# Kernel optimization log

Hardware: AMD Instinct MI355X
Metric: run time of the kernel (lower is better)

## Reference

```python
import jax, jax.numpy as jnp
import numpy as np

NUM_TYPES = 4
EPS = 1e-5
NEG_SLOPE = 0.01  # nn.LeakyReLU default


def hetero_linear(x, node_type, W, b):
    # x: [N, Cin], W: [T, Cin, Cout], b: [T, Cout]
    # Grouped GEMM via type-masked batched matmul (T is small and fixed).
    onehot = jax.nn.one_hot(node_type, NUM_TYPES, dtype=x.dtype)  # [N, T]
    xt = onehot.T[:, :, None] * x[None, :, :]                      # [T, N, Cin]
    y = jnp.einsum('tni,tio->no', xt, W)                           # [N, Cout]
    return y + b[node_type]


def hetero_batchnorm(x, node_type, gamma, beta):
    # Per-type batch statistics over the nodes of each type (training-mode BN).
    ones = jnp.ones((x.shape[0],), dtype=x.dtype)
    cnt = jax.ops.segment_sum(ones, node_type, num_segments=NUM_TYPES)      # [T]
    cnt = jnp.maximum(cnt, 1.0)
    s = jax.ops.segment_sum(x, node_type, num_segments=NUM_TYPES)           # [T, C]
    ss = jax.ops.segment_sum(x * x, node_type, num_segments=NUM_TYPES)      # [T, C]
    mean = s / cnt[:, None]
    var = ss / cnt[:, None] - mean * mean  # biased variance, as BN uses
    xn = (x - mean[node_type]) * jax.lax.rsqrt(var[node_type] + EPS)
    return xn * gamma[node_type] + beta[node_type]


def setup_inputs() -> dict:
    key = jax.random.key(0)
    ks = jax.random.split(key, 12)
    N, CIN, H, COUT, T = 32768, 256, 512, 256, NUM_TYPES
    x = jax.random.normal(ks[0], (N, CIN), dtype=jnp.float32)
    node_type = jax.random.randint(ks[1], (N,), 0, T, dtype=jnp.int32)
    def lin(k, ci, co):
        k1, k2 = jax.random.split(k)
        scale = 1.0 / np.sqrt(ci)
        W = jax.random.uniform(k1, (T, ci, co), jnp.float32, -scale, scale)
        b = jax.random.uniform(k2, (T, co), jnp.float32, -scale, scale)
        return W, b
    W1, b1 = lin(ks[2], CIN, H)
    W2, b2 = lin(ks[3], H, H)
    W3, b3 = lin(ks[4], H, COUT)
    gamma1 = jnp.ones((T, H), jnp.float32)
    beta1 = jnp.zeros((T, H), jnp.float32)
    gamma2 = jnp.ones((T, H), jnp.float32)
    beta2 = jnp.zeros((T, H), jnp.float32)
    return {"x": x, "node_type": node_type,
            "W1": W1, "b1": b1, "W2": W2, "b2": b2, "W3": W3, "b3": b3,
            "gamma1": gamma1, "beta1": beta1, "gamma2": gamma2, "beta2": beta2}


def reference(x, node_type, W1, b1, W2, b2, W3, b3, gamma1, beta1, gamma2, beta2):
    # Layer 1: HeteroLinear -> HeteroBatchNorm -> LeakyReLU (dropout p=0 -> identity)
    h = hetero_linear(x, node_type, W1, b1)
    h = hetero_batchnorm(h, node_type, gamma1, beta1)
    h = jax.nn.leaky_relu(h, NEG_SLOPE)
    # Layer 2
    h = hetero_linear(h, node_type, W2, b2)
    h = hetero_batchnorm(h, node_type, gamma2, beta2)
    h = jax.nn.leaky_relu(h, NEG_SLOPE)
    # Layer 3: plain_last -> no norm/act
    out = hetero_linear(h, node_type, W3, b3)
    return out
```

## Files before the change

### kernel.cpp

```cpp
#include <hip/hip_runtime.h>
#include <cstdint>
#include <cstddef>

#define N_NODES 32768
#define CIN 256
#define HDIM 512
#define COUT_F 256
#define NTYPE 4
#define ALIGN_SEG 128
#define NPAD (N_NODES + NTYPE * ALIGN_SEG)
#define BN_EPS 1e-5f
#define SLOPE 0.01f
#define NCHUNK 64

typedef unsigned short u16;
typedef __attribute__((ext_vector_type(8))) short bf16x8;
typedef __attribute__((ext_vector_type(4))) float f32x4;
typedef __attribute__((ext_vector_type(4))) u16 u16x4;

#define GLOBAL_AS __attribute__((address_space(1)))
#define LDS_AS __attribute__((address_space(3)))

__device__ __forceinline__ u16 f2bf(float f) {
  union { float f; unsigned u; } v{f};
  unsigned r = (v.u + 0x7FFF + ((v.u >> 16) & 1)) >> 16;
  return (u16)r;
}


__global__ void hist_kernel(const int* __restrict__ nt, int* __restrict__ blockHist) {
  __shared__ int h[NTYPE];
  int tid = threadIdx.x;
  if (tid < NTYPE) h[tid] = 0;
  __syncthreads();
  int i = blockIdx.x * 256 + tid;
  atomicAdd(&h[nt[i]], 1);
  __syncthreads();
  if (tid < NTYPE) blockHist[blockIdx.x * NTYPE + tid] = h[tid];
}

__global__ void scan_kernel(const int* __restrict__ blockHist, int* __restrict__ blockBase,
                            int* __restrict__ meta) {
  int tid = threadIdx.x;
  if (tid < NTYPE) {
    int run = 0;
    for (int b = 0; b < 128; ++b) {
      blockBase[b * NTYPE + tid] = run;
      run += blockHist[b * NTYPE + tid];
    }
    meta[tid] = run;
  }
  __syncthreads();
  if (tid == 0) {
    int s = 0;
    for (int t = 0; t < NTYPE; ++t) {
      meta[4 + t] = s;
      s += (meta[t] + ALIGN_SEG - 1) & ~(ALIGN_SEG - 1);
    }
    meta[8] = s;
  }
}

__global__ void rank_scatter_kernel(const int* __restrict__ nt, const int* __restrict__ blockBase,
                                    const int* __restrict__ meta, int* __restrict__ perm) {
  __shared__ int st[256];
  int tid = threadIdx.x;
  int i = blockIdx.x * 256 + tid;
  int t = nt[i];
  st[tid] = t;
  __syncthreads();
  int rank = 0;
  for (int j = 0; j < tid; ++j) rank += (st[j] == t) ? 1 : 0;
  perm[meta[4 + t] + blockBase[blockIdx.x * NTYPE + t] + rank] = i;
}

__global__ void gather_kernel(const float* __restrict__ x, const int* __restrict__ perm,
                              u16* __restrict__ xs) {
  int p = blockIdx.x;
  int src = perm[p];
  u16x4* dst = (u16x4*)(xs + (size_t)p * CIN);
  if (src < 0) {
    dst[threadIdx.x] = (u16x4)0;
  } else {
    float4 v = ((const float4*)(x + (size_t)src * CIN))[threadIdx.x];
    u16x4 o;
    o.x = f2bf(v.x); o.y = f2bf(v.y); o.z = f2bf(v.z); o.w = f2bf(v.w);
    dst[threadIdx.x] = o;
  }
}

template <int K, int COUT>
__global__ __launch_bounds__(256) void wtrans_kernel(const float* __restrict__ W,
                                                     u16* __restrict__ Wt) {
  const int t = blockIdx.z;
  const int k0 = blockIdx.x * 32, c0 = blockIdx.y * 32;
  const float* __restrict__ Ws = W + (size_t)t * K * COUT;
  u16* __restrict__ Wd = Wt + (size_t)t * COUT * K;
  __shared__ float tile[32][33];
  int tid = threadIdx.x;
#pragma unroll
  for (int p = 0; p < 4; ++p) {
    int idx = p * 256 + tid;
    int r = idx >> 5, c = idx & 31;
    tile[r][c] = Ws[(size_t)(k0 + r) * COUT + c0 + c];
  }
  __syncthreads();
#pragma unroll
  for (int p = 0; p < 4; ++p) {
    int idx = p * 256 + tid;
    int r = idx >> 5, c = idx & 31;
    Wd[(size_t)(c0 + r) * K + k0 + c] = f2bf(tile[c][r]);
  }
}


template <int K, int COUT, bool SCATTER>
__global__ __launch_bounds__(256) void mfma_gemm_kernel(
    const u16* __restrict__ A, const u16* __restrict__ Wt, const float* __restrict__ bias,
    float* __restrict__ Y, const int* __restrict__ meta, const int* __restrict__ perm) {
  const int col0 = blockIdx.x * 128, row0 = blockIdx.y * 128;
  const int s1 = meta[5], s2 = meta[6], s3 = meta[7];
  const int t = row0 >= s3 ? 3 : (row0 >= s2 ? 2 : (row0 >= s1 ? 1 : 0));
  const u16* __restrict__ Bt = Wt + (size_t)t * COUT * K;

  __shared__ __align__(16) u16 As[128 * 32];
  __shared__ __align__(16) u16 Bs[128 * 32];

  const int tid = threadIdx.x;
  const int wid = tid >> 6, lane = tid & 63;
  const int lr = lane & 15, ls = lane >> 4;
  const int wm = wid >> 1, wn = wid & 1;

  int a_off[4], b_off[4];
#pragma unroll
  for (int i = 0; i < 4; ++i) {
    int r = wm * 64 + i * 16 + lr;
    a_off[i] = r * 32 + (ls ^ ((r >> 1) & 3)) * 8;
  }
#pragma unroll
  for (int j = 0; j < 4; ++j) {
    int r = wn * 64 + j * 16 + lr;
    b_off[j] = r * 32 + (ls ^ ((r >> 1) & 3)) * 8;
  }

  int st_row[2], st_k[2];
#pragma unroll
  for (int p = 0; p < 2; ++p) {
    int c = p * 256 + tid;
    int r = c >> 2;
    int s = (c & 3) ^ ((r >> 1) & 3);
    st_row[p] = r;
    st_k[p] = s * 8;
  }
  const int lds_base0 = (tid & 192) * 8;

  f32x4 acc[4][4] = {};

  for (int k0 = 0; k0 < K; k0 += 32) {
#pragma unroll
    for (int p = 0; p < 2; ++p) {
      const u16* ga = A + (size_t)(row0 + st_row[p]) * K + k0 + st_k[p];
      const u16* gb = Bt + (size_t)(col0 + st_row[p]) * K + k0 + st_k[p];
      u16* la = As + p * 2048 + lds_base0;
      u16* lb = Bs + p * 2048 + lds_base0;
      __builtin_amdgcn_global_load_lds((const GLOBAL_AS void*)ga, (LDS_AS void*)la, 16, 0, 0);
      __builtin_amdgcn_global_load_lds((const GLOBAL_AS void*)gb, (LDS_AS void*)lb, 16, 0, 0);
    }
    __syncthreads();
    bf16x8 af[4], bfr[4];
#pragma unroll
    for (int i = 0; i < 4; ++i) af[i] = *(const bf16x8*)(As + a_off[i]);
#pragma unroll
    for (int j = 0; j < 4; ++j) bfr[j] = *(const bf16x8*)(Bs + b_off[j]);
#pragma unroll
    for (int i = 0; i < 4; ++i)
#pragma unroll
      for (int j = 0; j < 4; ++j)
        acc[i][j] = __builtin_amdgcn_mfma_f32_16x16x32_bf16(af[i], bfr[j], acc[i][j], 0, 0, 0);
    __syncthreads();
  }

  float bj[4];
#pragma unroll
  for (int j = 0; j < 4; ++j) bj[j] = bias[(size_t)t * COUT + col0 + wn * 64 + j * 16 + lr];

#pragma unroll
  for (int i = 0; i < 4; ++i) {
    int rbase = row0 + wm * 64 + i * 16 + ls * 4;
    if (SCATTER) {
      int dsts[4];
#pragma unroll
      for (int r = 0; r < 4; ++r) dsts[r] = perm[rbase + r];
#pragma unroll
      for (int j = 0; j < 4; ++j) {
        int gcol = col0 + wn * 64 + j * 16 + lr;
#pragma unroll
        for (int r = 0; r < 4; ++r) {
          if (dsts[r] >= 0) Y[(size_t)dsts[r] * COUT + gcol] = acc[i][j][r] + bj[j];
        }
      }
    } else {
#pragma unroll
      for (int j = 0; j < 4; ++j) {
        int gcol = col0 + wn * 64 + j * 16 + lr;
#pragma unroll
        for (int r = 0; r < 4; ++r) {
          Y[(size_t)(rbase + r) * COUT + gcol] = acc[i][j][r] + bj[j];
        }
      }
    }
  }
}


__global__ __launch_bounds__(256) void bn_partial_kernel(const float* __restrict__ h,
                                                         const int* __restrict__ meta,
                                                         float* __restrict__ partS,
                                                         float* __restrict__ partQ) {
  const int t = blockIdx.y;
  const int chunk = blockIdx.z;
  const int lane = threadIdx.x & 63;
  const int rl = threadIdx.x >> 6;
  const int c = blockIdx.x * 64 + lane;
  const int start = meta[4 + t];
  const int cnt = meta[t];
  float s = 0.f, q = 0.f;
  for (int r = chunk * 4 + rl; r < cnt; r += NCHUNK * 4) {
    float v = h[(size_t)(start + r) * HDIM + c];
    s += v;
    q += v * v;
  }
  __shared__ float redS[4][64], redQ[4][64];
  redS[rl][lane] = s;
  redQ[rl][lane] = q;
  __syncthreads();
  if (rl == 0) {
    float S = redS[0][lane] + redS[1][lane] + redS[2][lane] + redS[3][lane];
    float Q = redQ[0][lane] + redQ[1][lane] + redQ[2][lane] + redQ[3][lane];
    size_t o = ((size_t)t * NCHUNK + chunk) * HDIM + c;
    partS[o] = S;
    partQ[o] = Q;
  }
}

__global__ __launch_bounds__(256) void bn_finalize_kernel(const float* __restrict__ partS,
                                                          const float* __restrict__ partQ,
                                                          const int* __restrict__ meta,
                                                          float* __restrict__ mean,
                                                          float* __restrict__ rstd) {
  int idx = blockIdx.x * 256 + threadIdx.x;
  int t = idx >> 9;
  int c = idx & (HDIM - 1);
  float S = 0.f, Q = 0.f;
#pragma unroll 8
  for (int k = 0; k < NCHUNK; ++k) {
    size_t o = ((size_t)t * NCHUNK + k) * HDIM + c;
    S += partS[o];
    Q += partQ[o];
  }
  int cnt = meta[t];
  float n = (float)(cnt > 1 ? cnt : 1);
  float m = S / n;
  float var = Q / n - m * m;
  mean[idx] = m;
  rstd[idx] = rsqrtf(fmaxf(var, 0.f) + BN_EPS);
}

__global__ __launch_bounds__(256) void bn_apply_kernel(
    const float* __restrict__ h, const int* __restrict__ meta, const float* __restrict__ mean,
    const float* __restrict__ rstd, const float* __restrict__ gamma,
    const float* __restrict__ beta, u16* __restrict__ aout) {
  size_t idx = (size_t)blockIdx.x * 256 + threadIdx.x;
  int row = (int)(idx >> 7);
  int cq = (int)(idx & 127);
  const int s1 = meta[5], s2 = meta[6], s3 = meta[7];
  const int t = row >= s3 ? 3 : (row >= s2 ? 2 : (row >= s1 ? 1 : 0));
  float4 v = *(const float4*)(h + (size_t)row * HDIM + cq * 4);
  float4 m = *(const float4*)(mean + t * HDIM + cq * 4);
  float4 r = *(const float4*)(rstd + t * HDIM + cq * 4);
  float4 g = *(const float4*)(gamma + (size_t)t * HDIM + cq * 4);
  float4 b = *(const float4*)(beta + (size_t)t * HDIM + cq * 4);
  float o0 = (v.x - m.x) * r.x * g.x + b.x;
  float o1 = (v.y - m.y) * r.y * g.y + b.y;
  float o2 = (v.z - m.z) * r.z * g.z + b.z;
  float o3 = (v.w - m.w) * r.w * g.w + b.w;
  o0 = o0 >= 0.f ? o0 : SLOPE * o0;
  o1 = o1 >= 0.f ? o1 : SLOPE * o1;
  o2 = o2 >= 0.f ? o2 : SLOPE * o2;
  o3 = o3 >= 0.f ? o3 : SLOPE * o3;
  u16x4 o;
  o.x = f2bf(o0); o.y = f2bf(o1); o.z = f2bf(o2); o.w = f2bf(o3);
  *(u16x4*)(aout + (size_t)row * HDIM + cq * 4) = o;
}


extern "C" void kernel_launch(void* const* d_in, const int* in_sizes, int n_in, void* d_out,
                              int out_size, void* d_ws, size_t ws_size, hipStream_t stream) {
  const float* x = (const float*)d_in[0];
  const int* nt = (const int*)d_in[1];
  const float* W1 = (const float*)d_in[2];
  const float* b1 = (const float*)d_in[3];
  const float* W2 = (const float*)d_in[4];
  const float* b2 = (const float*)d_in[5];
  const float* W3 = (const float*)d_in[6];
  const float* b3 = (const float*)d_in[7];
  const float* g1 = (const float*)d_in[8];
  const float* be1 = (const float*)d_in[9];
  const float* g2 = (const float*)d_in[10];
  const float* be2 = (const float*)d_in[11];
  float* out = (float*)d_out;

  char* ws = (char*)d_ws;
  size_t off = 0;
  auto alloc = [&](size_t bytes) {
    void* p = ws + off;
    off = (off + bytes + 255) & ~(size_t)255;
    return p;
  };
  int* meta = (int*)alloc(16 * 4);
  int* blockHist = (int*)alloc(128 * NTYPE * 4);
  int* blockBase = (int*)alloc(128 * NTYPE * 4);
  int* perm = (int*)alloc((size_t)NPAD * 4);
  float* mean = (float*)alloc((size_t)NTYPE * HDIM * 4);
  float* rstd = (float*)alloc((size_t)NTYPE * HDIM * 4);
  float* partS = (float*)alloc((size_t)NTYPE * NCHUNK * HDIM * 4);
  float* partQ = (float*)alloc((size_t)NTYPE * NCHUNK * HDIM * 4);
  u16* Wt1 = (u16*)alloc((size_t)NTYPE * CIN * HDIM * 2);
  u16* Wt2 = (u16*)alloc((size_t)NTYPE * HDIM * HDIM * 2);
  u16* Wt3 = (u16*)alloc((size_t)NTYPE * HDIM * COUT_F * 2);
  u16* xs = (u16*)alloc((size_t)NPAD * CIN * 2);
  u16* abuf = (u16*)alloc((size_t)NPAD * HDIM * 2);
  float* hbuf = (float*)alloc((size_t)NPAD * HDIM * 4);

  hipMemsetAsync(meta, 0, 64, stream);
  hipMemsetAsync(perm, 0xFF, (size_t)NPAD * 4, stream);
  hist_kernel<<<128, 256, 0, stream>>>(nt, blockHist);
  scan_kernel<<<1, 64, 0, stream>>>(blockHist, blockBase, meta);
  rank_scatter_kernel<<<128, 256, 0, stream>>>(nt, blockBase, meta, perm);
  gather_kernel<<<NPAD, 64, 0, stream>>>(x, perm, xs);

  wtrans_kernel<CIN, HDIM><<<dim3(CIN / 32, HDIM / 32, NTYPE), 256, 0, stream>>>(W1, Wt1);
  wtrans_kernel<HDIM, HDIM><<<dim3(HDIM / 32, HDIM / 32, NTYPE), 256, 0, stream>>>(W2, Wt2);
  wtrans_kernel<HDIM, COUT_F><<<dim3(HDIM / 32, COUT_F / 32, NTYPE), 256, 0, stream>>>(W3, Wt3);

  mfma_gemm_kernel<CIN, HDIM, false>
      <<<dim3(HDIM / 128, NPAD / 128), 256, 0, stream>>>(xs, Wt1, b1, hbuf, meta, nullptr);
  bn_partial_kernel<<<dim3(HDIM / 64, NTYPE, NCHUNK), 256, 0, stream>>>(hbuf, meta, partS, partQ);
  bn_finalize_kernel<<<(NTYPE * HDIM) / 256, 256, 0, stream>>>(partS, partQ, meta, mean, rstd);
  bn_apply_kernel<<<(NPAD * (HDIM / 4)) / 256, 256, 0, stream>>>(hbuf, meta, mean, rstd, g1, be1,
                                                                 abuf);
  mfma_gemm_kernel<HDIM, HDIM, false>
      <<<dim3(HDIM / 128, NPAD / 128), 256, 0, stream>>>(abuf, Wt2, b2, hbuf, meta, nullptr);
  bn_partial_kernel<<<dim3(HDIM / 64, NTYPE, NCHUNK), 256, 0, stream>>>(hbuf, meta, partS, partQ);
  bn_finalize_kernel<<<(NTYPE * HDIM) / 256, 256, 0, stream>>>(partS, partQ, meta, mean, rstd);
  bn_apply_kernel<<<(NPAD * (HDIM / 4)) / 256, 256, 0, stream>>>(hbuf, meta, mean, rstd, g2, be2,
                                                                 abuf);
  mfma_gemm_kernel<HDIM, COUT_F, true>
      <<<dim3(COUT_F / 128, NPAD / 128), 256, 0, stream>>>(abuf, Wt3, b3, out, meta, perm);
}
```

Measured before the change: 190.1 us.

## Fuse BN statistics into GEMM epilogue, store bf16 hidden, widen K tile

Each GEMM epilogue now accumulates per-column sum and sum-of-squares for its 128-row block and reduces them through LDS into a per-row-block partial buffer. This removes the separate bn_partial pass over the hidden activations. The hidden activations are stored as bf16 instead of fp32, roughly halving the traffic for the write and for the BN apply read, at a small precision cost. The GEMM K step also grows from 32 to 64 with an 8-way XOR swizzle, giving fewer barriers per tile in exchange for more LDS per block.

```diff
diff --git a/kernel.cpp b/kernel.cpp
--- a/kernel.cpp
+++ b/kernel.cpp
@@ -9,9 +9,9 @@
 #define NTYPE 4
 #define ALIGN_SEG 128
 #define NPAD (N_NODES + NTYPE * ALIGN_SEG)
+#define NROWBLK (NPAD / 128)
 #define BN_EPS 1e-5f
 #define SLOPE 0.01f
-#define NCHUNK 64
 
 typedef unsigned short u16;
 typedef __attribute__((ext_vector_type(8))) short bf16x8;
@@ -25,6 +25,11 @@
   union { float f; unsigned u; } v{f};
   unsigned r = (v.u + 0x7FFF + ((v.u >> 16) & 1)) >> 16;
   return (u16)r;
+}
+__device__ __forceinline__ float bf2f(u16 b) {
+  union { unsigned u; float f; } v;
+  v.u = ((unsigned)b) << 16;
+  return v.f;
 }
 
 
@@ -114,69 +119,76 @@
 }
 
 
-template <int K, int COUT, bool SCATTER>
+template <int K, int COUT, bool SCATTER, bool STATS>
 __global__ __launch_bounds__(256) void mfma_gemm_kernel(
     const u16* __restrict__ A, const u16* __restrict__ Wt, const float* __restrict__ bias,
-    float* __restrict__ Y, const int* __restrict__ meta, const int* __restrict__ perm) {
+    u16* __restrict__ Yb, float* __restrict__ Yf, float* __restrict__ partS,
+    float* __restrict__ partQ, const int* __restrict__ meta, const int* __restrict__ perm) {
   const int col0 = blockIdx.x * 128, row0 = blockIdx.y * 128;
   const int s1 = meta[5], s2 = meta[6], s3 = meta[7];
   const int t = row0 >= s3 ? 3 : (row0 >= s2 ? 2 : (row0 >= s1 ? 1 : 0));
+  const int seg_end = meta[4 + t] + meta[t];
   const u16* __restrict__ Bt = Wt + (size_t)t * COUT * K;
 
-  __shared__ __align__(16) u16 As[128 * 32];
-  __shared__ __align__(16) u16 Bs[128 * 32];
+  __shared__ __align__(16) u16 As[128 * 64];
+  __shared__ __align__(16) u16 Bs[128 * 64];
 
   const int tid = threadIdx.x;
-  const int wid = tid >> 6, lane = tid & 63;
+  const int lane = tid & 63;
   const int lr = lane & 15, ls = lane >> 4;
+  const int wid = tid >> 6;
   const int wm = wid >> 1, wn = wid & 1;
 
-  int a_off[4], b_off[4];
+  int a_off[4][2], b_off[4][2];
 #pragma unroll
   for (int i = 0; i < 4; ++i) {
     int r = wm * 64 + i * 16 + lr;
-    a_off[i] = r * 32 + (ls ^ ((r >> 1) & 3)) * 8;
+#pragma unroll
+    for (int kk = 0; kk < 2; ++kk) a_off[i][kk] = r * 64 + (((kk * 4 + ls)) ^ (r & 7)) * 8;
   }
 #pragma unroll
   for (int j = 0; j < 4; ++j) {
     int r = wn * 64 + j * 16 + lr;
-    b_off[j] = r * 32 + (ls ^ ((r >> 1) & 3)) * 8;
-  }
-
-  int st_row[2], st_k[2];
-#pragma unroll
-  for (int p = 0; p < 2; ++p) {
-    int c = p * 256 + tid;
-    int r = c >> 2;
-    int s = (c & 3) ^ ((r >> 1) & 3);
+#pragma unroll
+    for (int kk = 0; kk < 2; ++kk) b_off[j][kk] = r * 64 + (((kk * 4 + ls)) ^ (r & 7)) * 8;
+  }
+
+  int st_row[4], st_col[4];
+#pragma unroll
+  for (int p = 0; p < 4; ++p) {
+    int l = p * 256 + tid;
+    int r = l >> 3, u = l & 7;
     st_row[p] = r;
-    st_k[p] = s * 8;
-  }
-  const int lds_base0 = (tid & 192) * 8;
+    st_col[p] = (u ^ (r & 7)) * 8;
+  }
+  const int lds_base = (tid & 192) * 8;
 
   f32x4 acc[4][4] = {};
 
-  for (int k0 = 0; k0 < K; k0 += 32) {
-#pragma unroll
-    for (int p = 0; p < 2; ++p) {
-      const u16* ga = A + (size_t)(row0 + st_row[p]) * K + k0 + st_k[p];
-      const u16* gb = Bt + (size_t)(col0 + st_row[p]) * K + k0 + st_k[p];
-      u16* la = As + p * 2048 + lds_base0;
-      u16* lb = Bs + p * 2048 + lds_base0;
-      __builtin_amdgcn_global_load_lds((const GLOBAL_AS void*)ga, (LDS_AS void*)la, 16, 0, 0);
-      __builtin_amdgcn_global_load_lds((const GLOBAL_AS void*)gb, (LDS_AS void*)lb, 16, 0, 0);
+  for (int k0 = 0; k0 < K; k0 += 64) {
+#pragma unroll
+    for (int p = 0; p < 4; ++p) {
+      const u16* ga = A + (size_t)(row0 + st_row[p]) * K + k0 + st_col[p];
+      const u16* gb = Bt + (size_t)(col0 + st_row[p]) * K + k0 + st_col[p];
+      __builtin_amdgcn_global_load_lds((const GLOBAL_AS void*)ga,
+                                       (LDS_AS void*)(As + p * 2048 + lds_base), 16, 0, 0);
+      __builtin_amdgcn_global_load_lds((const GLOBAL_AS void*)gb,
+                                       (LDS_AS void*)(Bs + p * 2048 + lds_base), 16, 0, 0);
     }
     __syncthreads();
-    bf16x8 af[4], bfr[4];
-#pragma unroll
-    for (int i = 0; i < 4; ++i) af[i] = *(const bf16x8*)(As + a_off[i]);
-#pragma unroll
-    for (int j = 0; j < 4; ++j) bfr[j] = *(const bf16x8*)(Bs + b_off[j]);
-#pragma unroll
-    for (int i = 0; i < 4; ++i)
-#pragma unroll
-      for (int j = 0; j < 4; ++j)
-        acc[i][j] = __builtin_amdgcn_mfma_f32_16x16x32_bf16(af[i], bfr[j], acc[i][j], 0, 0, 0);
+#pragma unroll
+    for (int kk = 0; kk < 2; ++kk) {
+      bf16x8 af[4], bfr[4];
+#pragma unroll
+      for (int i = 0; i < 4; ++i) af[i] = *(const bf16x8*)(As + a_off[i][kk]);
+#pragma unroll
+      for (int j = 0; j < 4; ++j) bfr[j] = *(const bf16x8*)(Bs + b_off[j][kk]);
+#pragma unroll
+      for (int i = 0; i < 4; ++i)
+#pragma unroll
+        for (int j = 0; j < 4; ++j)
+          acc[i][j] = __builtin_amdgcn_mfma_f32_16x16x32_bf16(af[i], bfr[j], acc[i][j], 0, 0, 0);
+    }
     __syncthreads();
   }
 
@@ -184,10 +196,10 @@
 #pragma unroll
   for (int j = 0; j < 4; ++j) bj[j] = bias[(size_t)t * COUT + col0 + wn * 64 + j * 16 + lr];
 
-#pragma unroll
-  for (int i = 0; i < 4; ++i) {
-    int rbase = row0 + wm * 64 + i * 16 + ls * 4;
-    if (SCATTER) {
+  if (SCATTER) {
+#pragma unroll
+    for (int i = 0; i < 4; ++i) {
+      int rbase = row0 + wm * 64 + i * 16 + ls * 4;
       int dsts[4];
 #pragma unroll
       for (int r = 0; r < 4; ++r) dsts[r] = perm[rbase + r];
@@ -196,52 +208,54 @@
         int gcol = col0 + wn * 64 + j * 16 + lr;
 #pragma unroll
         for (int r = 0; r < 4; ++r) {
-          if (dsts[r] >= 0) Y[(size_t)dsts[r] * COUT + gcol] = acc[i][j][r] + bj[j];
+          if (dsts[r] >= 0) Yf[(size_t)dsts[r] * COUT + gcol] = acc[i][j][r] + bj[j];
         }
       }
-    } else {
+    }
+  } else {
+    float s[4] = {}, q[4] = {};
+#pragma unroll
+    for (int i = 0; i < 4; ++i) {
+      int rbase = row0 + wm * 64 + i * 16 + ls * 4;
 #pragma unroll
       for (int j = 0; j < 4; ++j) {
         int gcol = col0 + wn * 64 + j * 16 + lr;
 #pragma unroll
         for (int r = 0; r < 4; ++r) {
-          Y[(size_t)(rbase + r) * COUT + gcol] = acc[i][j][r] + bj[j];
+          int row = rbase + r;
+          float y = acc[i][j][r] + bj[j];
+          Yb[(size_t)row * COUT + gcol] = f2bf(y);
+          if (STATS && row < seg_end) {
+            s[j] += y;
+            q[j] += y * y;
+          }
         }
       }
     }
-  }
-}
-
-
-__global__ __launch_bounds__(256) void bn_partial_kernel(const float* __restrict__ h,
-                                                         const int* __restrict__ meta,
-                                                         float* __restrict__ partS,
-                                                         float* __restrict__ partQ) {
-  const int t = blockIdx.y;
-  const int chunk = blockIdx.z;
-  const int lane = threadIdx.x & 63;
-  const int rl = threadIdx.x >> 6;
-  const int c = blockIdx.x * 64 + lane;
-  const int start = meta[4 + t];
-  const int cnt = meta[t];
-  float s = 0.f, q = 0.f;
-  for (int r = chunk * 4 + rl; r < cnt; r += NCHUNK * 4) {
-    float v = h[(size_t)(start + r) * HDIM + c];
-    s += v;
-    q += v * v;
-  }
-  __shared__ float redS[4][64], redQ[4][64];
-  redS[rl][lane] = s;
-  redQ[rl][lane] = q;
-  __syncthreads();
-  if (rl == 0) {
-    float S = redS[0][lane] + redS[1][lane] + redS[2][lane] + redS[3][lane];
-    float Q = redQ[0][lane] + redQ[1][lane] + redQ[2][lane] + redQ[3][lane];
-    size_t o = ((size_t)t * NCHUNK + chunk) * HDIM + c;
-    partS[o] = S;
-    partQ[o] = Q;
-  }
-}
+    if (STATS) {
+      float* sred = (float*)As;
+      float* qred = (float*)Bs;
+      int slot = (wm * 4 + ls) * 128 + wn * 64 + lr;
+#pragma unroll
+      for (int j = 0; j < 4; ++j) {
+        sred[slot + j * 16] = s[j];
+        qred[slot + j * 16] = q[j];
+      }
+      __syncthreads();
+      if (tid < 128) {
+        float S = 0.f, Q = 0.f;
+#pragma unroll
+        for (int k = 0; k < 8; ++k) {
+          S += sred[k * 128 + tid];
+          Q += qred[k * 128 + tid];
+        }
+        partS[(size_t)blockIdx.y * COUT + col0 + tid] = S;
+        partQ[(size_t)blockIdx.y * COUT + col0 + tid] = Q;
+      }
+    }
+  }
+}
+
 
 __global__ __launch_bounds__(256) void bn_finalize_kernel(const float* __restrict__ partS,
                                                           const float* __restrict__ partQ,
@@ -251,14 +265,15 @@
   int idx = blockIdx.x * 256 + threadIdx.x;
   int t = idx >> 9;
   int c = idx & (HDIM - 1);
+  int start = meta[4 + t];
+  int cnt = meta[t];
+  int b0 = start >> 7;
+  int nb = (cnt + 127) >> 7;
   float S = 0.f, Q = 0.f;
-#pragma unroll 8
-  for (int k = 0; k < NCHUNK; ++k) {
-    size_t o = ((size_t)t * NCHUNK + k) * HDIM + c;
-    S += partS[o];
-    Q += partQ[o];
-  }
-  int cnt = meta[t];
+  for (int b = 0; b < nb; ++b) {
+    S += partS[(size_t)(b0 + b) * HDIM + c];
+    Q += partQ[(size_t)(b0 + b) * HDIM + c];
+  }
   float n = (float)(cnt > 1 ? cnt : 1);
   float m = S / n;
   float var = Q / n - m * m;
@@ -266,31 +281,42 @@
   rstd[idx] = rsqrtf(fmaxf(var, 0.f) + BN_EPS);
 }
 
+
 __global__ __launch_bounds__(256) void bn_apply_kernel(
-    const float* __restrict__ h, const int* __restrict__ meta, const float* __restrict__ mean,
+    const u16* __restrict__ h, const int* __restrict__ meta, const float* __restrict__ mean,
     const float* __restrict__ rstd, const float* __restrict__ gamma,
     const float* __restrict__ beta, u16* __restrict__ aout) {
-  size_t idx = (size_t)blockIdx.x * 256 + threadIdx.x;
-  int row = (int)(idx >> 7);
-  int cq = (int)(idx & 127);
+  int idx = blockIdx.x * 256 + threadIdx.x;
+  int row = idx >> 6;
+  int g8 = (idx & 63) * 8;
   const int s1 = meta[5], s2 = meta[6], s3 = meta[7];
   const int t = row >= s3 ? 3 : (row >= s2 ? 2 : (row >= s1 ? 1 : 0));
-  float4 v = *(const float4*)(h + (size_t)row * HDIM + cq * 4);
-  float4 m = *(const float4*)(mean + t * HDIM + cq * 4);
-  float4 r = *(const float4*)(rstd + t * HDIM + cq * 4);
-  float4 g = *(const float4*)(gamma + (size_t)t * HDIM + cq * 4);
-  float4 b = *(const float4*)(beta + (size_t)t * HDIM + cq * 4);
-  float o0 = (v.x - m.x) * r.x * g.x + b.x;
-  float o1 = (v.y - m.y) * r.y * g.y + b.y;
-  float o2 = (v.z - m.z) * r.z * g.z + b.z;
-  float o3 = (v.w - m.w) * r.w * g.w + b.w;
-  o0 = o0 >= 0.f ? o0 : SLOPE * o0;
-  o1 = o1 >= 0.f ? o1 : SLOPE * o1;
-  o2 = o2 >= 0.f ? o2 : SLOPE * o2;
-  o3 = o3 >= 0.f ? o3 : SLOPE * o3;
-  u16x4 o;
-  o.x = f2bf(o0); o.y = f2bf(o1); o.z = f2bf(o2); o.w = f2bf(o3);
-  *(u16x4*)(aout + (size_t)row * HDIM + cq * 4) = o;
+  size_t base = (size_t)row * HDIM + g8;
+  uint4 v = *(const uint4*)(h + base);
+  unsigned w[4] = {v.x, v.y, v.z, v.w};
+  int tb = t * HDIM + g8;
+  float mv[8], rv[8], gv[8], bv[8];
+  *(float4*)&mv[0] = *(const float4*)(mean + tb);
+  *(float4*)&mv[4] = *(const float4*)(mean + tb + 4);
+  *(float4*)&rv[0] = *(const float4*)(rstd + tb);
+  *(float4*)&rv[4] = *(const float4*)(rstd + tb + 4);
+  *(float4*)&gv[0] = *(const float4*)(gamma + tb);
+  *(float4*)&gv[4] = *(const float4*)(gamma + tb + 4);
+  *(float4*)&bv[0] = *(const float4*)(beta + tb);
+  *(float4*)&bv[4] = *(const float4*)(beta + tb + 4);
+  unsigned o[4];
+#pragma unroll
+  for (int p = 0; p < 4; ++p) {
+    u16 lo = (u16)(w[p] & 0xFFFF), hi = (u16)(w[p] >> 16);
+    int e0 = p * 2, e1 = p * 2 + 1;
+    float sc0 = rv[e0] * gv[e0], sc1 = rv[e1] * gv[e1];
+    float y0 = bf2f(lo) * sc0 + (bv[e0] - mv[e0] * sc0);
+    float y1 = bf2f(hi) * sc1 + (bv[e1] - mv[e1] * sc1);
+    y0 = y0 >= 0.f ? y0 : SLOPE * y0;
+    y1 = y1 >= 0.f ? y1 : SLOPE * y1;
+    o[p] = (unsigned)f2bf(y0) | ((unsigned)f2bf(y1) << 16);
+  }
+  *(uint4*)(aout + base) = make_uint4(o[0], o[1], o[2], o[3]);
 }
 
 
@@ -323,14 +349,14 @@
   int* perm = (int*)alloc((size_t)NPAD * 4);
   float* mean = (float*)alloc((size_t)NTYPE * HDIM * 4);
   float* rstd = (float*)alloc((size_t)NTYPE * HDIM * 4);
-  float* partS = (float*)alloc((size_t)NTYPE * NCHUNK * HDIM * 4);
-  float* partQ = (float*)alloc((size_t)NTYPE * NCHUNK * HDIM * 4);
+  float* partS = (float*)alloc((size_t)NROWBLK * HDIM * 4);
+  float* partQ = (float*)alloc((size_t)NROWBLK * HDIM * 4);
   u16* Wt1 = (u16*)alloc((size_t)NTYPE * CIN * HDIM * 2);
   u16* Wt2 = (u16*)alloc((size_t)NTYPE * HDIM * HDIM * 2);
   u16* Wt3 = (u16*)alloc((size_t)NTYPE * HDIM * COUT_F * 2);
   u16* xs = (u16*)alloc((size_t)NPAD * CIN * 2);
   u16* abuf = (u16*)alloc((size_t)NPAD * HDIM * 2);
-  float* hbuf = (float*)alloc((size_t)NPAD * HDIM * 4);
+  u16* hb = (u16*)alloc((size_t)NPAD * HDIM * 2);
 
   hipMemsetAsync(meta, 0, 64, stream);
   hipMemsetAsync(perm, 0xFF, (size_t)NPAD * 4, stream);
@@ -343,18 +369,16 @@
   wtrans_kernel<HDIM, HDIM><<<dim3(HDIM / 32, HDIM / 32, NTYPE), 256, 0, stream>>>(W2, Wt2);
   wtrans_kernel<HDIM, COUT_F><<<dim3(HDIM / 32, COUT_F / 32, NTYPE), 256, 0, stream>>>(W3, Wt3);
 
-  mfma_gemm_kernel<CIN, HDIM, false>
-      <<<dim3(HDIM / 128, NPAD / 128), 256, 0, stream>>>(xs, Wt1, b1, hbuf, meta, nullptr);
-  bn_partial_kernel<<<dim3(HDIM / 64, NTYPE, NCHUNK), 256, 0, stream>>>(hbuf, meta, partS, partQ);
+  mfma_gemm_kernel<CIN, HDIM, false, true><<<dim3(HDIM / 128, NPAD / 128), 256, 0, stream>>>(
+      xs, Wt1, b1, hb, nullptr, partS, partQ, meta, nullptr);
   bn_finalize_kernel<<<(NTYPE * HDIM) / 256, 256, 0, stream>>>(partS, partQ, meta, mean, rstd);
-  bn_apply_kernel<<<(NPAD * (HDIM / 4)) / 256, 256, 0, stream>>>(hbuf, meta, mean, rstd, g1, be1,
+  bn_apply_kernel<<<(NPAD * (HDIM / 8)) / 256, 256, 0, stream>>>(hb, meta, mean, rstd, g1, be1,
                                                                  abuf);
-  mfma_gemm_kernel<HDIM, HDIM, false>
-      <<<dim3(HDIM / 128, NPAD / 128), 256, 0, stream>>>(abuf, Wt2, b2, hbuf, meta, nullptr);
-  bn_partial_kernel<<<dim3(HDIM / 64, NTYPE, NCHUNK), 256, 0, stream>>>(hbuf, meta, partS, partQ);
+  mfma_gemm_kernel<HDIM, HDIM, false, true><<<dim3(HDIM / 128, NPAD / 128), 256, 0, stream>>>(
+      abuf, Wt2, b2, hb, nullptr, partS, partQ, meta, nullptr);
   bn_finalize_kernel<<<(NTYPE * HDIM) / 256, 256, 0, stream>>>(partS, partQ, meta, mean, rstd);
-  bn_apply_kernel<<<(NPAD * (HDIM / 4)) / 256, 256, 0, stream>>>(hbuf, meta, mean, rstd, g2, be2,
+  bn_apply_kernel<<<(NPAD * (HDIM / 8)) / 256, 256, 0, stream>>>(hb, meta, mean, rstd, g2, be2,
                                                                  abuf);
-  mfma_gemm_kernel<HDIM, COUT_F, true>
-      <<<dim3(COUT_F / 128, NPAD / 128), 256, 0, stream>>>(abuf, Wt3, b3, out, meta, perm);
-}
+  mfma_gemm_kernel<HDIM, COUT_F, true, false><<<dim3(COUT_F / 128, NPAD / 128), 256, 0, stream>>>(
+      abuf, Wt3, b3, nullptr, out, nullptr, nullptr, meta, perm);
+}
```

New measurement: 194.8 us. 2.5% more time.
